# Kernel tuning notes

Hardware: AMD Instinct MI355X
Metric: run time of the kernel (lower is better)

## Reference

```python
import jax, jax.numpy as jnp
import numpy as np

B, C_IN, C_OUT, H, MAXN = 128, 32, 32, 4096, 6


def setup_inputs() -> dict:
    key = jax.random.key(0)
    ks = jax.random.split(key, 6)
    x = jax.random.normal(ks[0], (B, C_IN, H), dtype=jnp.float32)
    weight = jax.random.normal(ks[1], (C_OUT, C_IN, MAXN + 1), dtype=jnp.float32) * 0.05
    bias = jax.random.normal(ks[2], (C_OUT,), dtype=jnp.float32) * 0.05
    gamma = jnp.ones((C_OUT,), dtype=jnp.float32)
    beta = jnp.zeros((C_OUT,), dtype=jnp.float32)
    # hex neighbor table; -1 marks invalid (boundary) neighbors
    neighbors = jax.random.randint(ks[3], (H, MAXN), -1, H, dtype=jnp.int64)
    return {"x": x, "weight": weight, "bias": bias, "gamma": gamma,
            "beta": beta, "neighbors": neighbors, "groups": 1}


def reference(x, weight, bias, gamma, beta, neighbors, groups):
    Bsz, Cin, Hn = x.shape
    Cout, _, K = weight.shape  # K = total_inputs = max_neighbors + 1
    G = groups
    # global std normalization (torch std: unbiased, ddof=1)
    x = x / (jnp.std(x, ddof=1) + 1e-5)
    valid = (neighbors >= 0)                      # [H, K-1]
    idx = jnp.clip(neighbors, 0, None)
    nbr = x[:, :, idx] * valid.astype(x.dtype)[None, None]   # [B,C,H,K-1]
    allv = jnp.concatenate([x[..., None], nbr], axis=3)      # [B,C,H,K]
    allv = allv.reshape(Bsz, G, Cin // G, Hn, K)
    w = weight.reshape(G, Cout // G, Cin // G, K)
    out = jnp.einsum('bgihk,goik->bgoh', allv, w).reshape(Bsz, Cout, Hn)
    total_valid = valid.sum(axis=1).astype(out.dtype)[None, None] + 1.0  # [1,1,H]
    out = out / (total_valid + 1e-6)
    out = out + bias[None, :, None]
    # BatchNorm1d in training mode: per-channel over (batch, hex), biased var
    mean = out.mean(axis=(0, 2), keepdims=True)
    var = out.var(axis=(0, 2), keepdims=True)
    out = gamma[None, :, None] * (out - mean) * jax.lax.rsqrt(var + 1e-5) + beta[None, :, None]
    return out
```

## Files before the change

kernel.cpp:

```cpp
#include <hip/hip_runtime.h>
#include <stdint.h>
#include <stddef.h>

#define BSZ 128
#define CIN 32
#define COUT 32
#define HN 4096
#define K7 7
#define NTOT (BSZ*CIN*HN)
#define NBH  (BSZ*HN)

typedef __attribute__((ext_vector_type(8))) short short8;
typedef __attribute__((ext_vector_type(4))) float f32x4;
typedef __attribute__((ext_vector_type(4))) unsigned int u32x4;
typedef __attribute__((ext_vector_type(2))) unsigned int u32x2;

#define WS_OB   0
#define WS_WT   33554432
#define WS_NBR  33568768
#define WS_INVD 33699840
#define WS_OSTP 33716224
#define WS_OST  33781760

__device__ __forceinline__ unsigned short f32_to_bf16(float f){
    union { float f; uint32_t u; } v; v.f = f;
    uint32_t u = v.u;
    return (unsigned short)((u + 0x7FFFu + ((u >> 16) & 1u)) >> 16);
}
__device__ __forceinline__ float bf16_to_f32(unsigned short h){
    union { uint32_t u; float f; } v; v.u = ((uint32_t)h) << 16;
    return v.f;
}

__global__ void ktrans(const float* __restrict__ x,
                       unsigned short* __restrict__ xt,
                       const int* __restrict__ nbr,
                       const float* __restrict__ w,
                       int* __restrict__ nbr_pack,
                       float* __restrict__ invd,
                       unsigned short* __restrict__ wt,
                       float* __restrict__ ostatp){
    __shared__ float tile[32][260];
    int b  = blockIdx.x >> 4;
    int h0 = (blockIdx.x & 15) << 8;
    int t  = threadIdx.x;
    #pragma unroll
    for (int l = 0; l < 8; l++){
        int linear = l*256 + t;
        int c  = linear >> 6;
        int h4 = linear & 63;
        f32x4 v = __builtin_nontemporal_load(
            (const f32x4*)(x + ((size_t)(b*CIN + c))*HN + h0 + h4*4));
        *(f32x4*)&tile[c][h4*4] = v;
    }
    __syncthreads();
    int cg = (t & 3) * 8;
    int hw = t >> 2;
    #pragma unroll
    for (int r = 0; r < 4; r++){
        int h = r*64 + hw;
        alignas(16) unsigned short tmp[8];
        #pragma unroll
        for (int j = 0; j < 8; j++) tmp[j] = f32_to_bf16(tile[cg + j][h]);
        __builtin_nontemporal_store(*(const u32x4*)tmp,
            (u32x4*)(xt + ((size_t)(b*HN + h0 + h))*32 + cg));
    }
    if (blockIdx.x < 16){
        int h = blockIdx.x*256 + t;
        #pragma unroll
        for (int j = 0; j < 4; j++) ostatp[h*4 + j] = 0.0f;
        int cnt = 0;
        int pk[8];
        #pragma unroll
        for (int j = 0; j < 6; j++){
            int iv = nbr[h*6 + j];
            if (iv >= HN) iv = HN - 1;
            if (iv >= 0) cnt++; else iv = -1;
            pk[j] = iv;
        }
        pk[6] = cnt; pk[7] = 0;
        #pragma unroll
        for (int j = 0; j < 8; j++) nbr_pack[h*8 + j] = pk[j];
        invd[h] = 1.0f / ((float)cnt + 1.0f + 1e-6f);
    } else if (blockIdx.x == 16){
        for (int i = t; i < COUT*K7*CIN; i += 256){
            int o  = i / (K7*CIN);
            int kk = (i / CIN) % K7;
            int c  = i % CIN;
            wt[i] = f32_to_bf16(w[(o*CIN + c)*K7 + kk]);
        }
    }
}

__global__ __launch_bounds__(256) void kconv(
    const unsigned short* __restrict__ xt,
    const unsigned short* __restrict__ wt,
    const int* __restrict__ nbrp,
    const float* __restrict__ invd,
    unsigned short* __restrict__ ob,
    float* __restrict__ ostatp)
{
    __shared__ unsigned short otile[4][32][72];

    int lane = threadIdx.x & 63;
    int wv   = threadIdx.x >> 6;
    int n    = lane & 15;
    int quad = lane >> 4;
    int xcd  = blockIdx.x & 7;
    int j    = blockIdx.x >> 3;
    int b    = xcd*16 + (j >> 4);
    int hbase= ((j & 15)*4 + wv) * 64;

    short8 af[2][K7];
    #pragma unroll
    for (int mt = 0; mt < 2; mt++){
        int o = n + 16*mt;
        #pragma unroll
        for (int kk = 0; kk < K7; kk++)
            af[mt][kk] = *(const short8*)(wt + (size_t)(o*K7 + kk)*CIN + quad*8);
    }

    float sacc[8]  = {0,0,0,0,0,0,0,0};
    float sacc2[8] = {0,0,0,0,0,0,0,0};
    const short8 zero8 = {0,0,0,0,0,0,0,0};
    const unsigned short* xb = xt + (size_t)b*HN*CIN;

    int h = hbase + n;
    int4 na = *(const int4*)(nbrp + h*8);
    int4 nb = *(const int4*)(nbrp + h*8 + 4);
    float idv = invd[h];

    #pragma unroll 1
    for (int it = 0; it < 4; it++){
        int hn = hbase + (it < 3 ? it+1 : it)*16 + n;
        int4 na2 = *(const int4*)(nbrp + hn*8);
        int4 nb2 = *(const int4*)(nbrp + hn*8 + 4);
        float idv2 = invd[hn];

        int hc = hbase + it*16 + n;
        short8 bfr[K7];
        bfr[0] = *(const short8*)(xb + (size_t)hc*CIN + quad*8);
        int rows[6] = {na.x, na.y, na.z, na.w, nb.x, nb.y};
        #pragma unroll
        for (int kk = 0; kk < 6; kk++){
            int row  = rows[kk];
            int rowc = row < 0 ? 0 : row;
            bfr[kk+1] = *(const short8*)(xb + (size_t)rowc*CIN + quad*8);
            if (row < 0) bfr[kk+1] = zero8;
        }
        f32x4 acc0 = {0.f,0.f,0.f,0.f};
        f32x4 acc1 = {0.f,0.f,0.f,0.f};
        #pragma unroll
        for (int kk = 0; kk < K7; kk++){
            acc0 = __builtin_amdgcn_mfma_f32_16x16x32_bf16(af[0][kk], bfr[kk], acc0, 0, 0, 0);
            acc1 = __builtin_amdgcn_mfma_f32_16x16x32_bf16(af[1][kk], bfr[kk], acc1, 0, 0, 0);
        }
        #pragma unroll
        for (int mt = 0; mt < 2; mt++){
            f32x4 a = mt ? acc1 : acc0;
            #pragma unroll
            for (int r = 0; r < 4; r++){
                int o = mt*16 + quad*4 + r;
                float v = a[r]*idv;
                otile[wv][o][it*16 + n] = f32_to_bf16(v);
                sacc[mt*4 + r]  += v;
                sacc2[mt*4 + r] += v*v;
            }
        }
        na = na2; nb = nb2; idv = idv2;
    }

    #pragma unroll
    for (int ro = 0; ro < 4; ro++){
        int o  = ro*8 + (lane >> 3);
        int hh = (lane & 7)*8;
        u32x4 vv = *(const u32x4*)&otile[wv][o][hh];
        __builtin_nontemporal_store(vv,
            (u32x4*)(ob + ((size_t)(b*COUT + o))*HN + hbase + hh));
    }

    #pragma unroll
    for (int bit = 1; bit < 16; bit <<= 1){
        #pragma unroll
        for (int i = 0; i < 8; i++){
            sacc[i]  += __shfl_xor(sacc[i],  bit);
            sacc2[i] += __shfl_xor(sacc2[i], bit);
        }
    }
    if (n == 0){
        int slot = blockIdx.x & 255;
        #pragma unroll
        for (int mt = 0; mt < 2; mt++)
            #pragma unroll
            for (int r = 0; r < 4; r++){
                int o = mt*16 + quad*4 + r;
                atomicAdd(&ostatp[slot*64 + o],      sacc[mt*4 + r]);
                atomicAdd(&ostatp[slot*64 + 32 + o], sacc2[mt*4 + r]);
            }
    }
}

__global__ void kred(const float* __restrict__ ostatp,
                     float* __restrict__ ostat,
                     const float* __restrict__ gamma,
                     const float* __restrict__ beta){
    __shared__ float part[4][64];
    int t = threadIdx.x;
    int a = t & 63;
    int g = t >> 6;
    float s = 0.0f;
    #pragma unroll
    for (int j = 0; j < 64; j++)
        s += ostatp[(g*64 + j)*64 + a];
    part[g][a] = s;
    __syncthreads();
    if (t < 64)
        part[0][t] = part[0][t] + part[1][t] + part[2][t] + part[3][t];
    __syncthreads();
    if (t < 32){
        float mean = part[0][t]      * (1.0f/(float)NBH);
        float var  = part[0][32 + t] * (1.0f/(float)NBH) - mean*mean;
        float sc = gamma[t] * rsqrtf(var + 1e-5f);
        ostat[t]      = sc;
        ostat[32 + t] = beta[t] - mean*sc;
    }
}

__global__ void kbn(const unsigned short* __restrict__ ob,
                    float* __restrict__ out,
                    const float* __restrict__ ostat){
    __shared__ float sc[32], sh[32];
    int t = threadIdx.x;
    if (t < 32){ sc[t] = ostat[t]; sh[t] = ostat[32 + t]; }
    __syncthreads();
    int gid = blockIdx.x*256 + t;
    const u32x2* ob2 = (const u32x2*)ob;
    f32x4* out4 = (f32x4*)out;
    #pragma unroll
    for (int k = 0; k < 8; k++){
        int i = gid + k*(2048*256);
        int o = (i >> 10) & 31;
        u32x2 raw = __builtin_nontemporal_load(ob2 + i);
        const unsigned short* p = (const unsigned short*)&raw;
        float s = sc[o], bsh = sh[o];
        f32x4 r;
        r.x = bf16_to_f32(p[0])*s + bsh;
        r.y = bf16_to_f32(p[1])*s + bsh;
        r.z = bf16_to_f32(p[2])*s + bsh;
        r.w = bf16_to_f32(p[3])*s + bsh;
        __builtin_nontemporal_store(r, out4 + i);
    }
}

extern "C" void kernel_launch(void* const* d_in, const int* in_sizes, int n_in,
                              void* d_out, int out_size, void* d_ws, size_t ws_size,
                              hipStream_t stream) {
    const float* x      = (const float*)d_in[0];
    const float* weight = (const float*)d_in[1];
    const float* gamma  = (const float*)d_in[3];
    const float* beta   = (const float*)d_in[4];
    const int*   nbr    = (const int*)d_in[5];

    char* ws = (char*)d_ws;
    unsigned short* ob    = (unsigned short*)(ws + WS_OB);
    unsigned short* wt    = (unsigned short*)(ws + WS_WT);
    int*            nbrp  = (int*)(ws + WS_NBR);
    float*          invd  = (float*)(ws + WS_INVD);
    float*          ostatp= (float*)(ws + WS_OSTP);
    float*          ostat = (float*)(ws + WS_OST);
    float*          out   = (float*)d_out;
    unsigned short* xt    = (unsigned short*)d_out + 16777216;

    ktrans<<<2048, 256, 0, stream>>>(x, xt, nbr, weight, nbrp, invd, wt, ostatp);
    kconv <<<2048, 256, 0, stream>>>(xt, wt, nbrp, invd, ob, ostatp);
    kred  <<<1,    256, 0, stream>>>(ostatp, ostat, gamma, beta);
    kbn   <<<2048, 256, 0, stream>>>(ob, out, ostat);
}
```

Baseline: 190.9 us.

## Interleave batch pairs in transposed input so each gather serves two batches

The transposed bf16 input now places two batches side by side per hex row (64 channels per row). The conv kernel then processes a batch pair per block, reusing each neighbor index and weight fragment for two batches, and the grid is halved. Nontemporal loads and stores are replaced with ordinary accesses in the transpose, conv and BN kernels, and conv gets a launch-bounds occupancy hint. The aim is fewer index loads and better cache-line use on the gathers, at the cost of more registers and doubled LDS per block.

Result: faster. 184.8 us (-3.2%).

```diff
diff --git a/kernel.cpp b/kernel.cpp
--- a/kernel.cpp
+++ b/kernel.cpp
@@ -21,6 +21,7 @@
 #define WS_INVD 33699840
 #define WS_OSTP 33716224
 #define WS_OST  33781760
+
 
 __device__ __forceinline__ unsigned short f32_to_bf16(float f){
     union { float f; uint32_t u; } v; v.f = f;
@@ -41,29 +42,33 @@
                        unsigned short* __restrict__ wt,
                        float* __restrict__ ostatp){
     __shared__ float tile[32][260];
-    int b  = blockIdx.x >> 4;
+    int bp = blockIdx.x >> 4;
     int h0 = (blockIdx.x & 15) << 8;
     int t  = threadIdx.x;
-    #pragma unroll
-    for (int l = 0; l < 8; l++){
-        int linear = l*256 + t;
-        int c  = linear >> 6;
-        int h4 = linear & 63;
-        f32x4 v = __builtin_nontemporal_load(
-            (const f32x4*)(x + ((size_t)(b*CIN + c))*HN + h0 + h4*4));
-        *(f32x4*)&tile[c][h4*4] = v;
-    }
-    __syncthreads();
-    int cg = (t & 3) * 8;
-    int hw = t >> 2;
-    #pragma unroll
-    for (int r = 0; r < 4; r++){
-        int h = r*64 + hw;
-        alignas(16) unsigned short tmp[8];
-        #pragma unroll
-        for (int j = 0; j < 8; j++) tmp[j] = f32_to_bf16(tile[cg + j][h]);
-        __builtin_nontemporal_store(*(const u32x4*)tmp,
-            (u32x4*)(xt + ((size_t)(b*HN + h0 + h))*32 + cg));
+    #pragma unroll 1
+    for (int bb = 0; bb < 2; bb++){
+        int b = bp*2 + bb;
+        if (bb) __syncthreads();
+        #pragma unroll
+        for (int l = 0; l < 8; l++){
+            int linear = l*256 + t;
+            int c  = linear >> 6;
+            int h4 = linear & 63;
+            f32x4 v = *(const f32x4*)(x + ((size_t)(b*CIN + c))*HN + h0 + h4*4);
+            *(f32x4*)&tile[c][h4*4] = v;
+        }
+        __syncthreads();
+        int cg = (t & 3) * 8;
+        int hw = t >> 2;
+        #pragma unroll
+        for (int r = 0; r < 4; r++){
+            int h = r*64 + hw;
+            alignas(16) unsigned short tmp[8];
+            #pragma unroll
+            for (int j = 0; j < 8; j++) tmp[j] = f32_to_bf16(tile[cg + j][h]);
+            *(u32x4*)(xt + (size_t)bp*HN*64 + (size_t)(h0 + h)*64 + bb*32 + cg)
+                = *(const u32x4*)tmp;
+        }
     }
     if (blockIdx.x < 16){
         int h = blockIdx.x*256 + t;
@@ -92,7 +97,7 @@
     }
 }
 
-__global__ __launch_bounds__(256) void kconv(
+__global__ __launch_bounds__(256, 4) void kconv(
     const unsigned short* __restrict__ xt,
     const unsigned short* __restrict__ wt,
     const int* __restrict__ nbrp,
@@ -100,7 +105,7 @@
     unsigned short* __restrict__ ob,
     float* __restrict__ ostatp)
 {
-    __shared__ unsigned short otile[4][32][72];
+    __shared__ unsigned short otile[4][2][32][72];
 
     int lane = threadIdx.x & 63;
     int wv   = threadIdx.x >> 6;
@@ -108,7 +113,7 @@
     int quad = lane >> 4;
     int xcd  = blockIdx.x & 7;
     int j    = blockIdx.x >> 3;
-    int b    = xcd*16 + (j >> 4);
+    int bp   = xcd*8 + (j >> 4);
     int hbase= ((j & 15)*4 + wv) * 64;
 
     short8 af[2][K7];
@@ -123,7 +128,7 @@
     float sacc[8]  = {0,0,0,0,0,0,0,0};
     float sacc2[8] = {0,0,0,0,0,0,0,0};
     const short8 zero8 = {0,0,0,0,0,0,0,0};
-    const unsigned short* xb = xt + (size_t)b*HN*CIN;
+    const unsigned short* xb = xt + (size_t)bp*HN*64;
 
     int h = hbase + n;
     int4 na = *(const int4*)(nbrp + h*8);
@@ -138,45 +143,62 @@
         float idv2 = invd[hn];
 
         int hc = hbase + it*16 + n;
-        short8 bfr[K7];
-        bfr[0] = *(const short8*)(xb + (size_t)hc*CIN + quad*8);
+        short8 bfr[K7][2];
+        {
+            const unsigned short* rp = xb + (size_t)hc*64 + quad*8;
+            bfr[0][0] = *(const short8*)(rp);
+            bfr[0][1] = *(const short8*)(rp + 32);
+        }
         int rows[6] = {na.x, na.y, na.z, na.w, nb.x, nb.y};
         #pragma unroll
         for (int kk = 0; kk < 6; kk++){
             int row  = rows[kk];
             int rowc = row < 0 ? 0 : row;
-            bfr[kk+1] = *(const short8*)(xb + (size_t)rowc*CIN + quad*8);
-            if (row < 0) bfr[kk+1] = zero8;
-        }
-        f32x4 acc0 = {0.f,0.f,0.f,0.f};
-        f32x4 acc1 = {0.f,0.f,0.f,0.f};
+            const unsigned short* rp = xb + (size_t)rowc*64 + quad*8;
+            short8 v0 = *(const short8*)(rp);
+            short8 v1 = *(const short8*)(rp + 32);
+            if (row < 0){ v0 = zero8; v1 = zero8; }
+            bfr[kk+1][0] = v0;
+            bfr[kk+1][1] = v1;
+        }
+        f32x4 acc00 = {0.f,0.f,0.f,0.f};
+        f32x4 acc01 = {0.f,0.f,0.f,0.f};
+        f32x4 acc10 = {0.f,0.f,0.f,0.f};
+        f32x4 acc11 = {0.f,0.f,0.f,0.f};
         #pragma unroll
         for (int kk = 0; kk < K7; kk++){
-            acc0 = __builtin_amdgcn_mfma_f32_16x16x32_bf16(af[0][kk], bfr[kk], acc0, 0, 0, 0);
-            acc1 = __builtin_amdgcn_mfma_f32_16x16x32_bf16(af[1][kk], bfr[kk], acc1, 0, 0, 0);
-        }
-        #pragma unroll
-        for (int mt = 0; mt < 2; mt++){
-            f32x4 a = mt ? acc1 : acc0;
+            acc00 = __builtin_amdgcn_mfma_f32_16x16x32_bf16(af[0][kk], bfr[kk][0], acc00, 0, 0, 0);
+            acc01 = __builtin_amdgcn_mfma_f32_16x16x32_bf16(af[1][kk], bfr[kk][0], acc01, 0, 0, 0);
+            acc10 = __builtin_amdgcn_mfma_f32_16x16x32_bf16(af[0][kk], bfr[kk][1], acc10, 0, 0, 0);
+            acc11 = __builtin_amdgcn_mfma_f32_16x16x32_bf16(af[1][kk], bfr[kk][1], acc11, 0, 0, 0);
+        }
+        #pragma unroll
+        for (int p = 0; p < 2; p++){
             #pragma unroll
-            for (int r = 0; r < 4; r++){
-                int o = mt*16 + quad*4 + r;
-                float v = a[r]*idv;
-                otile[wv][o][it*16 + n] = f32_to_bf16(v);
-                sacc[mt*4 + r]  += v;
-                sacc2[mt*4 + r] += v*v;
+            for (int mt = 0; mt < 2; mt++){
+                f32x4 a = p ? (mt ? acc11 : acc10) : (mt ? acc01 : acc00);
+                #pragma unroll
+                for (int r = 0; r < 4; r++){
+                    int o = mt*16 + quad*4 + r;
+                    float v = a[r]*idv;
+                    otile[wv][p][o][it*16 + n] = f32_to_bf16(v);
+                    sacc[mt*4 + r]  += v;
+                    sacc2[mt*4 + r] += v*v;
+                }
             }
         }
         na = na2; nb = nb2; idv = idv2;
     }
 
     #pragma unroll
-    for (int ro = 0; ro < 4; ro++){
-        int o  = ro*8 + (lane >> 3);
-        int hh = (lane & 7)*8;
-        u32x4 vv = *(const u32x4*)&otile[wv][o][hh];
-        __builtin_nontemporal_store(vv,
-            (u32x4*)(ob + ((size_t)(b*COUT + o))*HN + hbase + hh));
+    for (int p = 0; p < 2; p++){
+        #pragma unroll
+        for (int ro = 0; ro < 4; ro++){
+            int o  = ro*8 + (lane >> 3);
+            int hh = (lane & 7)*8;
+            u32x4 vv = *(const u32x4*)&otile[wv][p][o][hh];
+            *(u32x4*)(ob + ((size_t)((bp*2 + p)*COUT + o))*HN + hbase + hh) = vv;
+        }
     }
 
     #pragma unroll
@@ -240,7 +262,7 @@
     for (int k = 0; k < 8; k++){
         int i = gid + k*(2048*256);
         int o = (i >> 10) & 31;
-        u32x2 raw = __builtin_nontemporal_load(ob2 + i);
+        u32x2 raw = *(ob2 + i);
         const unsigned short* p = (const unsigned short*)&raw;
         float s = sc[o], bsh = sh[o];
         f32x4 r;
@@ -248,7 +270,7 @@
         r.y = bf16_to_f32(p[1])*s + bsh;
         r.z = bf16_to_f32(p[2])*s + bsh;
         r.w = bf16_to_f32(p[3])*s + bsh;
-        __builtin_nontemporal_store(r, out4 + i);
+        *(out4 + i) = r;
     }
 }
 
@@ -271,8 +293,8 @@
     float*          out   = (float*)d_out;
     unsigned short* xt    = (unsigned short*)d_out + 16777216;
 
-    ktrans<<<2048, 256, 0, stream>>>(x, xt, nbr, weight, nbrp, invd, wt, ostatp);
-    kconv <<<2048, 256, 0, stream>>>(xt, wt, nbrp, invd, ob, ostatp);
+    ktrans<<<1024, 256, 0, stream>>>(x, xt, nbr, weight, nbrp, invd, wt, ostatp);
+    kconv <<<1024, 256, 0, stream>>>(xt, wt, nbrp, invd, ob, ostatp);
     kred  <<<1,    256, 0, stream>>>(ostatp, ostat, gamma, beta);
     kbn   <<<2048, 256, 0, stream>>>(ob, out, ostat);
 }
```
